# Performance work log

Measured on AMD Instinct MI355X. Metric: run time of the kernel, lower is better.

Reference implementation:

```python
import jax, jax.numpy as jnp
import numpy as np

B, S, IN, EMB, H = 4, 2048, 256, 512, 8
D = EMB // H
SCALE = 1.0 / np.sqrt(EMB)  # source uses 1/sqrt(embed_size), not head_dim
EPS = 1e-5


def setup_inputs() -> dict:
    key = jax.random.key(0)
    ks = jax.random.split(key, 20)
    def w(k, shape, fan_in):
        return jax.random.normal(k, shape, jnp.float32) * (1.0 / np.sqrt(fan_in))
    inp = {"state_emb": jax.random.normal(ks[0], (B, S, IN), jnp.float32)}
    i = 1
    for p in ("q", "k", "v"):
        inp[f"{p}_W1"] = w(ks[i], (IN, EMB), IN); i += 1
        inp[f"{p}_b1"] = jnp.zeros((EMB,), jnp.float32)
        inp[f"{p}_W2"] = w(ks[i], (EMB, EMB), EMB); i += 1
        inp[f"{p}_b2"] = jnp.zeros((EMB,), jnp.float32)
    inp["f_W1"] = w(ks[i], (EMB, 2 * EMB), EMB); i += 1
    inp["f_b1"] = jnp.zeros((2 * EMB,), jnp.float32)
    inp["f_W2"] = w(ks[i], (2 * EMB, EMB), 2 * EMB); i += 1
    inp["f_b2"] = jnp.zeros((EMB,), jnp.float32)
    inp["ln1_g"] = jnp.ones((EMB,), jnp.float32)
    inp["ln1_b"] = jnp.zeros((EMB,), jnp.float32)
    inp["ln2_g"] = jnp.ones((EMB,), jnp.float32)
    inp["ln2_b"] = jnp.zeros((EMB,), jnp.float32)
    return inp


def _mlp2(x, W1, b1, W2, b2):
    return jax.nn.relu(x @ W1 + b1) @ W2 + b2


def _layernorm(x, g, b):
    mu = jnp.mean(x, axis=-1, keepdims=True)
    var = jnp.mean(jnp.square(x - mu), axis=-1, keepdims=True)
    return (x - mu) * jax.lax.rsqrt(var + EPS) * g + b


def reference(state_emb, q_W1, q_b1, q_W2, q_b2, k_W1, k_b1, k_W2, k_b2,
              v_W1, v_b1, v_W2, v_b2, f_W1, f_b1, f_W2, f_b2,
              ln1_g, ln1_b, ln2_g, ln2_b):
    n, dim = state_emb.shape[0], state_emb.shape[1]
    q = _mlp2(state_emb, q_W1, q_b1, q_W2, q_b2)  # [n, dim, EMB]
    k = _mlp2(state_emb, k_W1, k_b1, k_W2, k_b2)
    v = _mlp2(state_emb, v_W1, v_b1, v_W2, v_b2)
    qh = q.reshape(n, dim, H, D)
    kh = k.reshape(n, dim, H, D)
    vh = v.reshape(n, dim, H, D)
    energy = jnp.einsum('nqhd,nkhd->nhqk', qh, kh)  # [n, H, dim, dim]
    attn = jax.nn.softmax(energy * SCALE, axis=-1)
    ctx = jnp.einsum('nhql,nlhd->nqhd', attn, vh).reshape(n, dim, EMB)
    x = _layernorm(ctx + q, ln1_g, ln1_b)  # residual with queries, per source
    ff = _mlp2(x, f_W1, f_b1, f_W2, f_b2)
    return _layernorm(x + ff, ln2_g, ln2_b)
```

## Files before the change

kernel.cpp:

```cpp
#include <hip/hip_runtime.h>
#include <hip/hip_bf16.h>
#include <math.h>

#define BB   4
#define SS   2048
#define INF_ 256
#define EMB  512
#define NH   8
#define HD   64
#define NT   8192

typedef unsigned short u16;
typedef unsigned int   u32;
typedef __attribute__((ext_vector_type(8))) short bf16x8;
typedef __attribute__((ext_vector_type(8))) unsigned short u16x8;
typedef __attribute__((ext_vector_type(4))) float f32x4;

constexpr float C2  = 0.06375871607f;
constexpr float RB  = 0.005624549f;
constexpr float TB  = 1.00390625f;
constexpr float EPS = 1e-5f;

__device__ __forceinline__ u16 f2bf(float v) {
    __hip_bfloat16 h = __float2bfloat16(v);
    return *(u16*)&h;
}
__device__ __forceinline__ float bf2f(u16 u) {
    __hip_bfloat16 h = *(__hip_bfloat16*)&u;
    return __bfloat162float(h);
}
__device__ __forceinline__ u16 ftrunc_bf(float v) {
    return (u16)(__float_as_uint(v * TB) >> 16);
}
__device__ __forceinline__ f32x4 mfma16(bf16x8 a, bf16x8 b, f32x4 c) {
    return __builtin_amdgcn_mfma_f32_16x16x32_bf16(a, b, c, 0, 0, 0);
}
__device__ __forceinline__ void async16(const void* g, void* l) {
    __builtin_amdgcn_global_load_lds(
        (const __attribute__((address_space(1))) void*)g,
        (__attribute__((address_space(3))) void*)l, 16, 0, 0);
}
__device__ __forceinline__ int derive_flag(const u16* x) {
    const int lane = threadIdx.x & 63;
    const unsigned e = (x[lane * 2] >> 7) & 0xFF;
    float pl = (e == 0 || (e >= 110 && e <= 140)) ? 1.0f : 0.0f;
    #pragma unroll
    for (int o = 1; o < 64; o <<= 1) pl += __shfl_xor(pl, o);
    return pl < 32.0f;
}

__global__ __launch_bounds__(256) void prep(
    const u16* __restrict__ xsrc,
    const void* w0, const void* w1, const void* w2, const void* w3,
    const void* w4, const void* w5, const void* w6, const void* w7,
    const void* p0, const void* p1, const void* p2, const void* p3,
    const void* p4, const void* p5, const void* p6, const void* p7,
    const void* p8, const void* p9, const void* p10, const void* p11,
    u16* __restrict__ xbf, u16* __restrict__ wt1, u16* __restrict__ wt2,
    u16* __restrict__ f1t, u16* __restrict__ f2t, float* __restrict__ small)
{
    const int isf = derive_flag(xsrc);
    const int z = blockIdx.z;
    const int tid = threadIdx.x;

    if (z < 8) {
        int K, M; const void* src; u16* dst;
        switch (z) {
            case 0: K=256;  M=512;  src=w0; dst=wt1;             break;
            case 1: K=256;  M=512;  src=w1; dst=wt1+512*256;     break;
            case 2: K=256;  M=512;  src=w2; dst=wt1+2*512*256;   break;
            case 3: K=512;  M=512;  src=w3; dst=wt2;             break;
            case 4: K=512;  M=512;  src=w4; dst=wt2+512*512;     break;
            case 5: K=512;  M=512;  src=w5; dst=wt2+2*512*512;   break;
            case 6: K=512;  M=1024; src=w6; dst=f1t;             break;
            default:K=1024; M=512;  src=w7; dst=f2t;             break;
        }
        const int m0 = blockIdx.x * 32, k0 = blockIdx.y * 32;
        if (m0 >= M || k0 >= K) return;
        __shared__ u16 t[32][33];
        const int tx = tid & 31, ty = tid >> 5;
        #pragma unroll
        for (int i = 0; i < 4; ++i) {
            const int kk = k0 + ty + i * 8;
            t[ty + i * 8][tx] = isf ? ftrunc_bf(((const float*)src)[(size_t)kk * M + m0 + tx])
                                    : ((const u16*)src)[(size_t)kk * M + m0 + tx];
        }
        __syncthreads();
        #pragma unroll
        for (int i = 0; i < 4; ++i) {
            const int mm = m0 + ty + i * 8;
            dst[(size_t)mm * K + k0 + tx] = t[tx][ty + i * 8];
        }
    } else if (z == 8) {
        const int bid = blockIdx.y * 32 + blockIdx.x;
        const int base = bid * 2048 + tid * 8;
        if (isf) {
            #pragma unroll
            for (int j = 0; j < 8; ++j)
                xbf[base + j] = ftrunc_bf(((const float*)xsrc)[base + j]);
        } else {
            *(u16x8*)&xbf[base] = *(const u16x8*)&xsrc[base];
        }
    } else {
        const int bid = blockIdx.y * 32 + blockIdx.x;
        if (bid >= 28) return;
        const int e = bid * 256 + tid;
        int id, i;
        if (e < 3072)      { id = e >> 9;               i = e & 511;          }
        else if (e < 4096) { id = 6;                    i = e - 3072;         }
        else               { id = 7 + ((e - 4096) >> 9); i = (e - 4096) & 511; }
        const void* src;
        switch (id) {
            case 0: src = p0; break;  case 1: src = p1; break;
            case 2: src = p2; break;  case 3: src = p3; break;
            case 4: src = p4; break;  case 5: src = p5; break;
            case 6: src = p6; break;  case 7: src = p7; break;
            case 8: src = p8; break;  case 9: src = p9; break;
            case 10: src = p10; break; default: src = p11; break;
        }
        small[e] = isf ? ((const float*)src)[i] : bf2f(((const u16*)src)[i]);
    }
}

template <int TR, int TC, bool RELU, bool AWHICH, bool VOUT>
__global__ __launch_bounds__(256) void gemm_bt(
    const u16* __restrict__ Aall, const u16* __restrict__ Wtall,
    const float* __restrict__ ball, u16* __restrict__ out,
    u16* __restrict__ vtb, int N, int K, int M)
{
    constexpr int RT = TR / 32, CT = TC / 32;
    constexpr int AR = TR / 32, BR = TC / 32;
    __shared__ __align__(16) u16 sA[2][TR * 64];
    __shared__ __align__(16) u16 sB[2][TC * 64];

    const int mtiles = M / TC;
    const int which = blockIdx.x / mtiles;
    const int colb  = blockIdx.x % mtiles;
    const int row0 = blockIdx.y * TR, col0 = colb * TC;
    const u16* A  = Aall + (AWHICH ? (size_t)which * N * K : 0);
    const u16* Wt = Wtall + (size_t)which * M * K;
    const float* bias = ball + (size_t)which * M;

    const int tid = threadIdx.x;
    const int lane = tid & 63, w = tid >> 6;
    const int wrow = (w & 1) * (TR / 2), wcol = (w >> 1) * (TC / 2);
    const int c = lane & 15, quad = lane >> 4;

    const u16* ap[AR]; const u16* bp[BR];
    #pragma unroll
    for (int i = 0; i < AR; ++i) {
        const int raw = i * 256 + tid, r = raw >> 3, ch = (raw & 7) ^ (r & 7);
        ap[i] = A + (size_t)(row0 + r) * K + ch * 8;
    }
    #pragma unroll
    for (int i = 0; i < BR; ++i) {
        const int raw = i * 256 + tid, r = raw >> 3, ch = (raw & 7) ^ (r & 7);
        bp[i] = Wt + (size_t)(col0 + r) * K + ch * 8;
    }
    auto stage = [&](int buf) {
        #pragma unroll
        for (int i = 0; i < AR; ++i) {
            async16(ap[i], (char*)&sA[buf][0] + (i * 256 + tid) * 16);
            ap[i] += 64;
        }
        #pragma unroll
        for (int i = 0; i < BR; ++i) {
            async16(bp[i], (char*)&sB[buf][0] + (i * 256 + tid) * 16);
            bp[i] += 64;
        }
    };
    stage(0);

    f32x4 acc[RT][CT] = {};
    const int nIter = K >> 6;

    for (int t = 0; t < nIter; ++t) {
        __syncthreads();
        const int buf = t & 1;
        if (t + 1 < nIter) stage(buf ^ 1);

        #pragma unroll
        for (int kt = 0; kt < 2; ++kt) {
            bf16x8 af[RT], bfr[CT];
            #pragma unroll
            for (int rt = 0; rt < RT; ++rt) {
                const int r = wrow + rt * 16 + c;
                af[rt] = *(const bf16x8*)&sA[buf][(r * 8 + ((kt * 4 + quad) ^ (r & 7))) * 8];
            }
            #pragma unroll
            for (int ct = 0; ct < CT; ++ct) {
                const int r = wcol + ct * 16 + c;
                bfr[ct] = *(const bf16x8*)&sB[buf][(r * 8 + ((kt * 4 + quad) ^ (r & 7))) * 8];
            }
            #pragma unroll
            for (int rt = 0; rt < RT; ++rt)
                #pragma unroll
                for (int ct = 0; ct < CT; ++ct)
                    acc[rt][ct] = mfma16(af[rt], bfr[ct], acc[rt][ct]);
        }
    }

    if (VOUT && which == 2) {
        u16* smem = &sA[0][0];
        __syncthreads();
        #pragma unroll
        for (int rt = 0; rt < RT; ++rt) {
            const int rowb = wrow + rt * 16 + quad * 4;
            #pragma unroll
            for (int ct = 0; ct < CT; ++ct) {
                const int col = wcol + ct * 16 + c;
                const float bb = bias[col0 + col];
                ushort4 pk;
                pk.x = ftrunc_bf(acc[rt][ct][0] + bb);
                pk.y = ftrunc_bf(acc[rt][ct][1] + bb);
                pk.z = ftrunc_bf(acc[rt][ct][2] + bb);
                pk.w = ftrunc_bf(acc[rt][ct][3] + bb);
                *(ushort4*)&smem[col * 136 + rowb] = pk;
            }
        }
        __syncthreads();
        const int dcol = tid >> 2, part = tid & 3;
        const int hg = (col0 + dcol) >> 6, dd = (col0 + dcol) & 63;
        const int bb = row0 >> 11, s0 = row0 & 2047;
        u16* dst = vtb + ((size_t)(bb * NH + hg) * HD + dd) * SS + s0 + part * 32;
        #pragma unroll
        for (int j = 0; j < 4; ++j)
            *(u16x8*)&dst[j * 8] = *(const u16x8*)&smem[dcol * 136 + part * 32 + j * 8];
        return;
    }

    const size_t outW = (size_t)which * N * M;
    #pragma unroll
    for (int rt = 0; rt < RT; ++rt) {
        #pragma unroll
        for (int i = 0; i < 4; ++i) {
            const int row = row0 + wrow + rt * 16 + quad * 4 + i;
            #pragma unroll
            for (int ct = 0; ct < CT; ++ct) {
                const int col = col0 + wcol + ct * 16 + c;
                float v = acc[rt][ct][i] + bias[col];
                if (RELU) v = fmaxf(v, 0.0f);
                out[outW + (size_t)row * M + col] = ftrunc_bf(v);
            }
        }
    }
}

__global__ __launch_bounds__(256) void attn_mfma(
    const u16* __restrict__ q, const u16* __restrict__ k,
    const u16* __restrict__ vt, u16* __restrict__ ctx)
{
    __shared__ __align__(16) u16 sK[2][64 * 64];
    __shared__ __align__(16) u16 sV[2][64 * 64];

    const int tid = threadIdx.x;
    const int w = tid >> 6, lane = tid & 63;
    const int c = lane & 15, quad = lane >> 4;
    const int id = blockIdx.x;
    const int slot = id >> 3;
    const int bh = ((id & 7) << 2) | (slot >> 5);
    const int qt = slot & 31;
    const int b = bh >> 3, h = bh & 7;
    const int q0 = qt * 64;
    const size_t tokbase = (size_t)b * SS;
    const int hoff = h * HD;

    const int myq = q0 + w * 16 + c;
    bf16x8 qf[2];
    #pragma unroll
    for (int kt = 0; kt < 2; ++kt)
        qf[kt] = *(const bf16x8*)&q[(tokbase + myq) * EMB + hoff + kt * 32 + quad * 8];

    const u16* kp[2]; const u16* vp[2];
    #pragma unroll
    for (int i = 0; i < 2; ++i) {
        const int raw = i * 256 + tid, rr = raw >> 3, ch = (raw & 7) ^ (rr & 7);
        kp[i] = k + (tokbase + rr) * EMB + hoff + ch * 8;
        vp[i] = vt + ((size_t)(b * NH + h) * HD + rr) * SS + ch * 8;
    }
    auto stage = [&](int buf) {
        #pragma unroll
        for (int i = 0; i < 2; ++i) {
            async16(kp[i], (char*)&sK[buf][0] + (i * 256 + tid) * 16);
            kp[i] += 64 * EMB;
        }
        #pragma unroll
        for (int i = 0; i < 2; ++i) {
            async16(vp[i], (char*)&sV[buf][0] + (i * 256 + tid) * 16);
            vp[i] += 64;
        }
    };
    stage(0);

    const int addr0 = (c + 16 * ((quad & 1) * 2)) * 4;
    const int addr1 = addr0 + 64;

    float l_lane = 0.0f;
    f32x4 accO[4] = {};

    for (int t = 0; t < SS / 64; ++t) {
        __syncthreads();
        const int buf = t & 1;
        if (t + 1 < SS / 64) stage(buf ^ 1);

        f32x4 accS[4] = {};
        #pragma unroll
        for (int mt = 0; mt < 4; ++mt) {
            const int key = mt * 16 + c;
            #pragma unroll
            for (int kt = 0; kt < 2; ++kt) {
                bf16x8 kf = *(const bf16x8*)&sK[buf][(key * 8 + ((kt * 4 + quad) ^ (key & 7))) * 8];
                accS[mt] = mfma16(kf, qf[kt], accS[mt]);
            }
        }

        u32 pw[8];
        float ls = 0.0f;
        #pragma unroll
        for (int mt = 0; mt < 4; ++mt) {
            const float e0 = __builtin_amdgcn_exp2f(fmaf(accS[mt][0], C2, RB));
            const float e1 = __builtin_amdgcn_exp2f(fmaf(accS[mt][1], C2, RB));
            const float e2 = __builtin_amdgcn_exp2f(fmaf(accS[mt][2], C2, RB));
            const float e3 = __builtin_amdgcn_exp2f(fmaf(accS[mt][3], C2, RB));
            ls += (e0 + e1) + (e2 + e3);
            pw[2 * mt]     = __builtin_amdgcn_perm(__float_as_uint(e1), __float_as_uint(e0), 0x07060302u);
            pw[2 * mt + 1] = __builtin_amdgcn_perm(__float_as_uint(e3), __float_as_uint(e2), 0x07060302u);
        }
        l_lane += ls;

        #pragma unroll
        for (int kt = 0; kt < 2; ++kt) {
            const int m = (quad >> 1) + 2 * kt;
            union { u32 u[4]; bf16x8 v; } pb;
            pb.u[0] = (u32)__builtin_amdgcn_ds_bpermute(addr0, (int)pw[2 * m]);
            pb.u[1] = (u32)__builtin_amdgcn_ds_bpermute(addr0, (int)pw[2 * m + 1]);
            pb.u[2] = (u32)__builtin_amdgcn_ds_bpermute(addr1, (int)pw[2 * m]);
            pb.u[3] = (u32)__builtin_amdgcn_ds_bpermute(addr1, (int)pw[2 * m + 1]);
            #pragma unroll
            for (int nt = 0; nt < 4; ++nt) {
                const int d = nt * 16 + c;
                bf16x8 vf = *(const bf16x8*)&sV[buf][(d * 8 + ((kt * 4 + quad) ^ (d & 7))) * 8];
                accO[nt] = mfma16(vf, pb.v, accO[nt]);
            }
        }
    }

    float l = l_lane;
    l += __shfl_xor(l, 16);
    l += __shfl_xor(l, 32);
    const float li = (l > 0.0f) ? (1.0f / l) : 0.0f;

    const int tok = q0 + w * 16 + c;
    u16* dst = ctx + (tokbase + tok) * EMB + hoff + quad * 4;
    #pragma unroll
    for (int nt = 0; nt < 4; ++nt) {
        ushort4 pk;
        pk.x = ftrunc_bf(accO[nt][0] * li);
        pk.y = ftrunc_bf(accO[nt][1] * li);
        pk.z = ftrunc_bf(accO[nt][2] * li);
        pk.w = ftrunc_bf(accO[nt][3] * li);
        *(ushort4*)&dst[nt * 16] = pk;
    }
}

__global__ __launch_bounds__(256) void ln_mid(
    const u16* __restrict__ a, const u16* __restrict__ b2,
    const float* __restrict__ g, const float* __restrict__ be,
    u16* __restrict__ outb)
{
    const int wave = threadIdx.x >> 6, lane = threadIdx.x & 63;
    const size_t row = (size_t)blockIdx.x * 4 + wave;
    const u16x8 av = *(const u16x8*)&a[row * EMB + lane * 8];
    const u16x8 bv = *(const u16x8*)&b2[row * EMB + lane * 8];
    float vals[8], sum = 0.0f;
    #pragma unroll
    for (int i = 0; i < 8; ++i) { vals[i] = bf2f(av[i]) + bf2f(bv[i]); sum += vals[i]; }
    #pragma unroll
    for (int o = 1; o < 64; o <<= 1) sum += __shfl_xor(sum, o);
    const float mu = sum * (1.0f / 512.0f);
    float vs = 0.0f;
    #pragma unroll
    for (int i = 0; i < 8; ++i) { const float d = vals[i] - mu; vs += d * d; }
    #pragma unroll
    for (int o = 1; o < 64; o <<= 1) vs += __shfl_xor(vs, o);
    const float rstd = rsqrtf(vs * (1.0f / 512.0f) + EPS);
    u16x8 ov;
    #pragma unroll
    for (int i = 0; i < 8; ++i) {
        const int col = lane * 8 + i;
        ov[i] = f2bf((vals[i] - mu) * rstd * g[col] + be[col]);
    }
    *(u16x8*)&outb[row * EMB + lane * 8] = ov;
}

__global__ __launch_bounds__(256) void ln_final(
    const u16* __restrict__ a, const u16* __restrict__ b2,
    const float* __restrict__ g, const float* __restrict__ be,
    void* __restrict__ dout, const u16* __restrict__ xsrc)
{
    const int isf = derive_flag(xsrc);
    const int wave = threadIdx.x >> 6, lane = threadIdx.x & 63;
    const size_t row = (size_t)blockIdx.x * 4 + wave;
    const u16x8 av = *(const u16x8*)&a[row * EMB + lane * 8];
    const u16x8 bv = *(const u16x8*)&b2[row * EMB + lane * 8];
    float vals[8], sum = 0.0f;
    #pragma unroll
    for (int i = 0; i < 8; ++i) { vals[i] = bf2f(av[i]) + bf2f(bv[i]); sum += vals[i]; }
    #pragma unroll
    for (int o = 1; o < 64; o <<= 1) sum += __shfl_xor(sum, o);
    const float mu = sum * (1.0f / 512.0f);
    float vs = 0.0f;
    #pragma unroll
    for (int i = 0; i < 8; ++i) { const float d = vals[i] - mu; vs += d * d; }
    #pragma unroll
    for (int o = 1; o < 64; o <<= 1) vs += __shfl_xor(vs, o);
    const float rstd = rsqrtf(vs * (1.0f / 512.0f) + EPS);
    if (isf) {
        #pragma unroll
        for (int i = 0; i < 8; ++i) {
            const int col = lane * 8 + i;
            ((float*)dout)[row * EMB + col] = (vals[i] - mu) * rstd * g[col] + be[col];
        }
    } else {
        u16x8 ov;
        #pragma unroll
        for (int i = 0; i < 8; ++i) {
            const int col = lane * 8 + i;
            ov[i] = f2bf((vals[i] - mu) * rstd * g[col] + be[col]);
        }
        *(u16x8*)&((u16*)dout)[row * EMB + lane * 8] = ov;
    }
}

extern "C" void kernel_launch(void* const* d_in, const int* in_sizes, int n_in,
                              void* d_out, int out_size, void* d_ws, size_t ws_size,
                              hipStream_t stream)
{
    char* ws = (char*)d_ws;
    float* small = (float*)(ws + 0);
    u16*   wt1   = (u16*)(ws + 32768);
    u16*   wt2   = (u16*)(ws + 819200);
    u16*   f1t   = (u16*)(ws + 2392064);
    u16*   f2t   = (u16*)(ws + 3440640);
    u16*   xbf   = (u16*)(ws + 4489216);
    u16*   h3    = (u16*)(ws + 8683520);
    u16*   qkv   = (u16*)(ws + 33849344);
    u16*   vtb   = (u16*)(ws + 59015168);
    u16*   ctxb  = (u16*)(ws + 67403776);
    u16*   x1b   = (u16*)(ws + 75792384);
    u16*   ffb   = (u16*)(ws + 84180992);

    const dim3 blk(256);
    const u16* xsrc = (const u16*)d_in[0];

    prep<<<dim3(32, 32, 10), blk, 0, stream>>>(
        xsrc,
        d_in[1], d_in[5], d_in[9], d_in[3], d_in[7], d_in[11], d_in[13], d_in[15],
        d_in[2], d_in[6], d_in[10], d_in[4], d_in[8], d_in[12],
        d_in[14], d_in[16], d_in[17], d_in[18], d_in[19], d_in[20],
        xbf, wt1, wt2, f1t, f2t, small);

    gemm_bt<128, 64, true, false, false><<<dim3(24, 64), blk, 0, stream>>>(
        xbf, wt1, small + 0, h3, nullptr, NT, INF_, EMB);
    gemm_bt<128, 64, false, true, true><<<dim3(24, 64), blk, 0, stream>>>(
        h3, wt2, small + 1536, qkv, vtb, NT, EMB, EMB);

    attn_mfma<<<dim3(1024), blk, 0, stream>>>(
        qkv, qkv + (size_t)NT * EMB, vtb, ctxb);

    ln_mid<<<NT / 4, blk, 0, stream>>>(ctxb, qkv, small + 4608, small + 5120, x1b);

    u16* h2 = h3;
    gemm_bt<128, 64, true, false, false><<<dim3(16, 64), blk, 0, stream>>>(
        x1b, f1t, small + 3072, h2, nullptr, NT, EMB, 1024);
    gemm_bt<128, 64, false, false, false><<<dim3(8, 64), blk, 0, stream>>>(
        h2, f2t, small + 4096, ffb, nullptr, NT, 1024, EMB);

    ln_final<<<NT / 4, blk, 0, stream>>>(x1b, ffb, small + 5632, small + 6144, d_out, xsrc);
}
```

Before: 273.5 us.

## Use single-buffered 128x128 GEMM tiles and LDS-based P transpose in attention

The GEMM drops double buffering for a single shared-memory stage with a sync after loading, which shrinks LDS use so larger 128x128 tiles fit. Three of the four GEMM launches move to 128-column tiles, and the V-transpose epilogue is reworked to match. In attention, the ds_bpermute shuffle of the softmax probabilities is replaced by a per-wave LDS round trip. This trades load/compute overlap and extra LDS traffic for more reuse per tile and fewer blocks.

```diff
diff --git a/kernel.cpp b/kernel.cpp
--- a/kernel.cpp
+++ b/kernel.cpp
@@ -130,8 +130,11 @@
 {
     constexpr int RT = TR / 32, CT = TC / 32;
     constexpr int AR = TR / 32, BR = TC / 32;
-    __shared__ __align__(16) u16 sA[2][TR * 64];
-    __shared__ __align__(16) u16 sB[2][TC * 64];
+    constexpr int SSTAGE = (TR + TC) * 64;
+    constexpr int SELEMS = VOUT ? (SSTAGE > TC * 136 ? SSTAGE : TC * 136) : SSTAGE;
+    __shared__ __align__(16) u16 smem[SELEMS];
+    u16* sA = smem;
+    u16* sB = smem + TR * 64;
 
     const int mtiles = M / TC;
     const int which = blockIdx.x / mtiles;
@@ -157,27 +160,22 @@
         const int raw = i * 256 + tid, r = raw >> 3, ch = (raw & 7) ^ (r & 7);
         bp[i] = Wt + (size_t)(col0 + r) * K + ch * 8;
     }
-    auto stage = [&](int buf) {
+
+    f32x4 acc[RT][CT] = {};
+
+    for (int k0 = 0; k0 < K; k0 += 64) {
+        __syncthreads();
         #pragma unroll
         for (int i = 0; i < AR; ++i) {
-            async16(ap[i], (char*)&sA[buf][0] + (i * 256 + tid) * 16);
+            async16(ap[i], (char*)sA + (i * 256 + tid) * 16);
             ap[i] += 64;
         }
         #pragma unroll
         for (int i = 0; i < BR; ++i) {
-            async16(bp[i], (char*)&sB[buf][0] + (i * 256 + tid) * 16);
+            async16(bp[i], (char*)sB + (i * 256 + tid) * 16);
             bp[i] += 64;
         }
-    };
-    stage(0);
-
-    f32x4 acc[RT][CT] = {};
-    const int nIter = K >> 6;
-
-    for (int t = 0; t < nIter; ++t) {
-        __syncthreads();
-        const int buf = t & 1;
-        if (t + 1 < nIter) stage(buf ^ 1);
+        __syncthreads();
 
         #pragma unroll
         for (int kt = 0; kt < 2; ++kt) {
@@ -185,12 +183,12 @@
             #pragma unroll
             for (int rt = 0; rt < RT; ++rt) {
                 const int r = wrow + rt * 16 + c;
-                af[rt] = *(const bf16x8*)&sA[buf][(r * 8 + ((kt * 4 + quad) ^ (r & 7))) * 8];
+                af[rt] = *(const bf16x8*)&sA[(r * 8 + ((kt * 4 + quad) ^ (r & 7))) * 8];
             }
             #pragma unroll
             for (int ct = 0; ct < CT; ++ct) {
                 const int r = wcol + ct * 16 + c;
-                bfr[ct] = *(const bf16x8*)&sB[buf][(r * 8 + ((kt * 4 + quad) ^ (r & 7))) * 8];
+                bfr[ct] = *(const bf16x8*)&sB[(r * 8 + ((kt * 4 + quad) ^ (r & 7))) * 8];
             }
             #pragma unroll
             for (int rt = 0; rt < RT; ++rt)
@@ -201,7 +199,6 @@
     }
 
     if (VOUT && which == 2) {
-        u16* smem = &sA[0][0];
         __syncthreads();
         #pragma unroll
         for (int rt = 0; rt < RT; ++rt) {
@@ -219,13 +216,13 @@
             }
         }
         __syncthreads();
-        const int dcol = tid >> 2, part = tid & 3;
-        const int hg = (col0 + dcol) >> 6, dd = (col0 + dcol) & 63;
+        const int dl = tid >> 1, half = tid & 1;
+        const int hg = (col0 + dl) >> 6, dd = (col0 + dl) & 63;
         const int bb = row0 >> 11, s0 = row0 & 2047;
-        u16* dst = vtb + ((size_t)(bb * NH + hg) * HD + dd) * SS + s0 + part * 32;
-        #pragma unroll
-        for (int j = 0; j < 4; ++j)
-            *(u16x8*)&dst[j * 8] = *(const u16x8*)&smem[dcol * 136 + part * 32 + j * 8];
+        u16* dst = vtb + ((size_t)(bb * NH + hg) * HD + dd) * SS + s0 + half * 64;
+        #pragma unroll
+        for (int j = 0; j < 8; ++j)
+            *(u16x8*)&dst[j * 8] = *(const u16x8*)&smem[dl * 136 + half * 64 + j * 8];
         return;
     }
 
@@ -252,6 +249,7 @@
 {
     __shared__ __align__(16) u16 sK[2][64 * 64];
     __shared__ __align__(16) u16 sV[2][64 * 64];
+    __shared__ __align__(16) u16 sP[4][16 * 64];
 
     const int tid = threadIdx.x;
     const int w = tid >> 6, lane = tid & 63;
@@ -292,9 +290,6 @@
     };
     stage(0);
 
-    const int addr0 = (c + 16 * ((quad & 1) * 2)) * 4;
-    const int addr1 = addr0 + 64;
-
     float l_lane = 0.0f;
     f32x4 accO[4] = {};
 
@@ -329,18 +324,24 @@
         l_lane += ls;
 
         #pragma unroll
-        for (int kt = 0; kt < 2; ++kt) {
-            const int m = (quad >> 1) + 2 * kt;
-            union { u32 u[4]; bf16x8 v; } pb;
-            pb.u[0] = (u32)__builtin_amdgcn_ds_bpermute(addr0, (int)pw[2 * m]);
-            pb.u[1] = (u32)__builtin_amdgcn_ds_bpermute(addr0, (int)pw[2 * m + 1]);
-            pb.u[2] = (u32)__builtin_amdgcn_ds_bpermute(addr1, (int)pw[2 * m]);
-            pb.u[3] = (u32)__builtin_amdgcn_ds_bpermute(addr1, (int)pw[2 * m + 1]);
-            #pragma unroll
-            for (int nt = 0; nt < 4; ++nt) {
-                const int d = nt * 16 + c;
+        for (int mt = 0; mt < 4; ++mt) {
+            const int chunkW = 2 * mt + (quad >> 1);
+            const int blk = c * 8 + (chunkW ^ (c & 7));
+            uint2 u; u.x = pw[2 * mt]; u.y = pw[2 * mt + 1];
+            *(uint2*)((char*)&sP[w][0] + blk * 16 + 8 * (quad & 1)) = u;
+        }
+
+        bf16x8 pf[2];
+        #pragma unroll
+        for (int kt = 0; kt < 2; ++kt)
+            pf[kt] = *(const bf16x8*)&sP[w][(c * 8 + ((kt * 4 + quad) ^ (c & 7))) * 8];
+        #pragma unroll
+        for (int nt = 0; nt < 4; ++nt) {
+            const int d = nt * 16 + c;
+            #pragma unroll
+            for (int kt = 0; kt < 2; ++kt) {
                 bf16x8 vf = *(const bf16x8*)&sV[buf][(d * 8 + ((kt * 4 + quad) ^ (d & 7))) * 8];
-                accO[nt] = mfma16(vf, pb.v, accO[nt]);
+                accO[nt] = mfma16(vf, pf[kt], accO[nt]);
             }
         }
     }
@@ -460,9 +461,9 @@
         d_in[14], d_in[16], d_in[17], d_in[18], d_in[19], d_in[20],
         xbf, wt1, wt2, f1t, f2t, small);
 
-    gemm_bt<128, 64, true, false, false><<<dim3(24, 64), blk, 0, stream>>>(
+    gemm_bt<128, 128, true, false, false><<<dim3(12, 64), blk, 0, stream>>>(
         xbf, wt1, small + 0, h3, nullptr, NT, INF_, EMB);
-    gemm_bt<128, 64, false, true, true><<<dim3(24, 64), blk, 0, stream>>>(
+    gemm_bt<128, 128, false, true, true><<<dim3(12, 64), blk, 0, stream>>>(
         h3, wt2, small + 1536, qkv, vtb, NT, EMB, EMB);
 
     attn_mfma<<<dim3(1024), blk, 0, stream>>>(
@@ -471,7 +472,7 @@
     ln_mid<<<NT / 4, blk, 0, stream>>>(ctxb, qkv, small + 4608, small + 5120, x1b);
 
     u16* h2 = h3;
-    gemm_bt<128, 64, true, false, false><<<dim3(16, 64), blk, 0, stream>>>(
+    gemm_bt<128, 128, true, false, false><<<dim3(8, 64), blk, 0, stream>>>(
         x1b, f1t, small + 3072, h2, nullptr, NT, EMB, 1024);
     gemm_bt<128, 64, false, false, false><<<dim3(8, 64), blk, 0, stream>>>(
         h2, f2t, small + 4096, ffb, nullptr, NT, 1024, EMB);
```

Measured after the change: 259.3 us. 5.2% less time.
